# Performance work log

Measured on AMD Instinct MI355X. Metric: run time of the kernel, lower is better.

Reference implementation:

```python
import jax, jax.numpy as jnp
import numpy as np

B, S, D, H, DH = 1, 4096, 768, 12, 64
BS = 64            # block size
NB = S // BS       # 64 blocks
R = 3              # random blocks per query block
L = 2              # encoder layers
V = 50358          # vocab
F = 3072           # ffn hidden
C = 8              # num labels
EPS = 1e-12


def _ln(x, w, b):
    mu = jnp.mean(x, -1, keepdims=True)
    var = jnp.var(x, -1, keepdims=True)
    return (x - mu) * jax.lax.rsqrt(var + EPS) * w + b


def _bigbird_attn(x, rand, Wq, bq, Wk, bk, Wv, bv, Wo, bo):
    # x: [B,S,D]; rand: [H,NB,R] int block indices
    def split(h):  # -> [B,H,NB,BS,DH]
        return h.reshape(B, NB, BS, H, DH).transpose(0, 3, 1, 2, 4)
    q = split(x @ Wq + bq)
    k = split(x @ Wk + bk)
    v = split(x @ Wv + bv)
    scale = 1.0 / np.sqrt(DH).astype(np.float32)
    kf = k.reshape(B, H, S, DH)
    vf = v.reshape(B, H, S, DH)
    # global (first/last) query blocks attend to everything
    qe = q[:, :, jnp.array([0, NB - 1])]                       # [B,H,2,BS,DH]
    se = jnp.einsum('bhnqd,bhkd->bhnqk', qe, kf) * scale       # [B,H,2,BS,S]
    oe = jnp.einsum('bhnqk,bhkd->bhnqd', jax.nn.softmax(se, -1), vf)
    # middle query blocks: global(0, NB-1) + sliding window + R random blocks
    mid = jnp.arange(1, NB - 1)                                # [M]
    win = jnp.stack([jnp.zeros_like(mid), jnp.full_like(mid, NB - 1),
                     mid - 1, mid, mid + 1], -1)               # [M,5]
    band = jnp.concatenate([jnp.broadcast_to(win, (H, NB - 2, 5)),
                            rand[:, 1:NB - 1]], -1)            # [H,M,W]
    Wn = band.shape[-1]
    hidx = jnp.arange(H)[:, None, None]
    kb = k[:, hidx, band].reshape(B, H, NB - 2, Wn * BS, DH)
    vb = v[:, hidx, band].reshape(B, H, NB - 2, Wn * BS, DH)
    sm = jnp.einsum('bhmqd,bhmkd->bhmqk', q[:, :, 1:NB - 1], kb) * scale
    om = jnp.einsum('bhmqk,bhmkd->bhmqd', jax.nn.softmax(sm, -1), vb)
    o = jnp.concatenate([oe[:, :, 0:1], om, oe[:, :, 1:2]], 2)  # [B,H,NB,BS,DH]
    o = o.transpose(0, 2, 3, 1, 4).reshape(B, S, D)
    return o @ Wo + bo


def _forward(input_ids, rand_attn, word_emb, pos_emb, emb_ln_w, emb_ln_b,
             Wq, bq, Wk, bk, Wv, bv, Wo, bo, ln1_w, ln1_b,
             W1, b1, W2, b2, ln2_w, ln2_b, Wc, bc):
    h = word_emb[input_ids] + pos_emb[None, :S]
    h = _ln(h, emb_ln_w, emb_ln_b)
    for l in range(L):
        a = _bigbird_attn(h, rand_attn[l], Wq[l], bq[l], Wk[l], bk[l],
                          Wv[l], bv[l], Wo[l], bo[l])
        h = _ln(h + a, ln1_w[l], ln1_b[l])
        f = jax.nn.gelu(h @ W1[l] + b1[l], approximate=True) @ W2[l] + b2[l]
        h = _ln(h + f, ln2_w[l], ln2_b[l])
    return h[:, -1, :] @ Wc + bc   # [B, C]


def setup_inputs() -> dict:
    key = jax.random.key(0)
    ks = jax.random.split(key, 24)
    std = 0.02
    d = {
        'input_ids': jax.random.randint(ks[0], (B, S), 0, V, dtype=jnp.int32),
        'rand_attn': jax.random.randint(ks[1], (L, H, NB, R), 0, NB, dtype=jnp.int32),
        'word_emb': jax.random.normal(ks[2], (V, D), jnp.float32) * std,
        'pos_emb': jax.random.normal(ks[3], (S, D), jnp.float32) * std,
        'emb_ln_w': jnp.ones((D,), jnp.float32),
        'emb_ln_b': jnp.zeros((D,), jnp.float32),
        'Wq': jax.random.normal(ks[4], (L, D, D), jnp.float32) * std,
        'bq': jnp.zeros((L, D), jnp.float32),
        'Wk': jax.random.normal(ks[5], (L, D, D), jnp.float32) * std,
        'bk': jnp.zeros((L, D), jnp.float32),
        'Wv': jax.random.normal(ks[6], (L, D, D), jnp.float32) * std,
        'bv': jnp.zeros((L, D), jnp.float32),
        'Wo': jax.random.normal(ks[7], (L, D, D), jnp.float32) * std,
        'bo': jnp.zeros((L, D), jnp.float32),
        'ln1_w': jnp.ones((L, D), jnp.float32),
        'ln1_b': jnp.zeros((L, D), jnp.float32),
        'W1': jax.random.normal(ks[8], (L, D, F), jnp.float32) * std,
        'b1': jnp.zeros((L, F), jnp.float32),
        'W2': jax.random.normal(ks[9], (L, F, D), jnp.float32) * std,
        'b2': jnp.zeros((L, D), jnp.float32),
        'ln2_w': jnp.ones((L, D), jnp.float32),
        'ln2_b': jnp.zeros((L, D), jnp.float32),
        'Wc': jax.random.normal(ks[10], (D, C), jnp.float32) * std,
        'bc': jnp.zeros((C,), jnp.float32),
    }
    return d


def reference(input_ids, rand_attn, word_emb, pos_emb, emb_ln_w, emb_ln_b,
              Wq, bq, Wk, bk, Wv, bv, Wo, bo, ln1_w, ln1_b,
              W1, b1, W2, b2, ln2_w, ln2_b, Wc, bc):
    return _forward(input_ids, rand_attn, word_emb, pos_emb, emb_ln_w, emb_ln_b,
                    Wq, bq, Wk, bk, Wv, bv, Wo, bo, ln1_w, ln1_b,
                    W1, b1, W2, b2, ln2_w, ln2_b, Wc, bc)
```

## Files before the change

kernel.cpp:

```cpp
#include <hip/hip_runtime.h>
#include <stdint.h>

#define S_LEN 4096
#define DMODEL 768
#define NHEAD 12
#define DHEAD 64
#define NBLK 64
#define FF 3072
#define NLAYER 2
#define NMID (NHEAD * (NBLK - 2))
#define NEDGE_WG (NHEAD * 2 * 8)

typedef __attribute__((ext_vector_type(8))) short short8;
typedef __attribute__((ext_vector_type(4))) float floatx4;
typedef unsigned short ushort_t;

__device__ __forceinline__ unsigned short f2bf(float f) {
    union { float f; unsigned u; } v; v.f = f;
    unsigned r = v.u + 0x7FFFu + ((v.u >> 16) & 1u);
    return (unsigned short)(r >> 16);
}

__device__ __forceinline__ void load_lds16(const void* g, void* l) {
    __builtin_amdgcn_global_load_lds((const __attribute__((address_space(1))) void*)g,
                                     (__attribute__((address_space(3))) void*)l, 16, 0, 0);
}

__global__ void embed_ln_kernel(const int* __restrict__ ids, const float* __restrict__ wemb,
                                const float* __restrict__ pemb, const float* __restrict__ w,
                                const float* __restrict__ b, float* __restrict__ hf,
                                ushort_t* __restrict__ hb) {
    int s = blockIdx.x, t = threadIdx.x;
    const float* we = wemb + (size_t)ids[s] * DMODEL;
    const float* pe = pemb + (size_t)s * DMODEL;
    float x0 = we[t] + pe[t];
    float x1 = we[t + 256] + pe[t + 256];
    float x2 = we[t + 512] + pe[t + 512];
    float sum = x0 + x1 + x2;
    float sum2 = x0 * x0 + x1 * x1 + x2 * x2;
    __shared__ float sred[8];
    for (int o = 32; o >= 1; o >>= 1) { sum += __shfl_down(sum, o); sum2 += __shfl_down(sum2, o); }
    if ((t & 63) == 0) { sred[t >> 6] = sum; sred[4 + (t >> 6)] = sum2; }
    __syncthreads();
    float ts = sred[0] + sred[1] + sred[2] + sred[3];
    float ts2 = sred[4] + sred[5] + sred[6] + sred[7];
    float mu = ts * (1.0f / DMODEL);
    float rs = rsqrtf(ts2 * (1.0f / DMODEL) - mu * mu + 1e-12f);
    size_t base = (size_t)s * DMODEL;
    float y0 = (x0 - mu) * rs * w[t] + b[t];
    float y1 = (x1 - mu) * rs * w[t + 256] + b[t + 256];
    float y2 = (x2 - mu) * rs * w[t + 512] + b[t + 512];
    hf[base + t] = y0; hf[base + t + 256] = y1; hf[base + t + 512] = y2;
    hb[base + t] = f2bf(y0); hb[base + t + 256] = f2bf(y1); hb[base + t + 512] = f2bf(y2);
}

__global__ void ln_kernel(const float* __restrict__ in, const float* __restrict__ w,
                          const float* __restrict__ b, float* __restrict__ hf,
                          ushort_t* __restrict__ hb) {
    int s = blockIdx.x, t = threadIdx.x;
    const float* row = in + (size_t)s * DMODEL;
    float x0 = row[t], x1 = row[t + 256], x2 = row[t + 512];
    float sum = x0 + x1 + x2;
    float sum2 = x0 * x0 + x1 * x1 + x2 * x2;
    __shared__ float sred[8];
    for (int o = 32; o >= 1; o >>= 1) { sum += __shfl_down(sum, o); sum2 += __shfl_down(sum2, o); }
    if ((t & 63) == 0) { sred[t >> 6] = sum; sred[4 + (t >> 6)] = sum2; }
    __syncthreads();
    float ts = sred[0] + sred[1] + sred[2] + sred[3];
    float ts2 = sred[4] + sred[5] + sred[6] + sred[7];
    float mu = ts * (1.0f / DMODEL);
    float rs = rsqrtf(ts2 * (1.0f / DMODEL) - mu * mu + 1e-12f);
    size_t base = (size_t)s * DMODEL;
    float y0 = (x0 - mu) * rs * w[t] + b[t];
    float y1 = (x1 - mu) * rs * w[t + 256] + b[t + 256];
    float y2 = (x2 - mu) * rs * w[t + 512] + b[t + 512];
    hf[base + t] = y0; hf[base + t + 256] = y1; hf[base + t + 512] = y2;
    hb[base + t] = f2bf(y0); hb[base + t + 256] = f2bf(y1); hb[base + t + 512] = f2bf(y2);
}

__global__ void transpose_cvt(const float* __restrict__ src, ushort_t* __restrict__ dst,
                              int K, int N) {
    __shared__ float tile[32][33];
    int n0 = blockIdx.x * 32, k0 = blockIdx.y * 32;
    int tx = threadIdx.x, ty = threadIdx.y;
    for (int i = 0; i < 32; i += 8)
        tile[ty + i][tx] = src[(size_t)(k0 + ty + i) * N + n0 + tx];
    __syncthreads();
    for (int i = 0; i < 32; i += 8)
        dst[(size_t)(n0 + ty + i) * K + k0 + tx] = f2bf(tile[tx][ty + i]);
}

template <int MODE>
__global__ __launch_bounds__(256, 2) void gemm_bf16(
    const ushort_t* __restrict__ A, const ushort_t* __restrict__ BT,
    int M, int N, int K,
    const float* __restrict__ bias, const float* __restrict__ resid,
    float* __restrict__ outf, ushort_t* __restrict__ outb,
    ushort_t* __restrict__ qout, ushort_t* __restrict__ kout, ushort_t* __restrict__ vout,
    const float* __restrict__ bq, const float* __restrict__ bk, const float* __restrict__ bv) {
    __shared__ __align__(16) ushort_t Asm[128 * 32];
    __shared__ __align__(16) ushort_t Bsm[128 * 32];
    int tid = threadIdx.x;
    int lane = tid & 63, wave = tid >> 6;
    int quad = lane >> 4, l16 = lane & 15;
    int wm = wave >> 1, wn = wave & 1;
    long arow0 = (long)blockIdx.y * 128;
    long bcol0 = (long)blockIdx.x * 128;
    int rr = lane >> 2;
    int gchunk = (lane & 3) ^ (rr & 3) ^ ((rr >> 2) & 3);
    const ushort_t* agp0 = A + (arow0 + rr) * (long)K + gchunk * 8;
    const ushort_t* bgp0 = BT + (bcol0 + rr) * (long)K + gchunk * 8;
    int sl = quad ^ (l16 & 3) ^ ((l16 >> 2) & 3);
    floatx4 acc[4][4];
#pragma unroll
    for (int i = 0; i < 4; i++)
#pragma unroll
        for (int j = 0; j < 4; j++) acc[i][j] = (floatx4){0.f, 0.f, 0.f, 0.f};

    for (int k0 = 0; k0 < K; k0 += 32) {
        __syncthreads();
#pragma unroll
        for (int t2 = 0; t2 < 2; t2++) {
            int seg = wave * 2 + t2;
            load_lds16(agp0 + (long)seg * 16 * K + k0, Asm + seg * 512);
            load_lds16(bgp0 + (long)seg * 16 * K + k0, Bsm + seg * 512);
        }
        __syncthreads();
        short8 af[4], bfv[4];
#pragma unroll
        for (int i = 0; i < 4; i++)
            af[i] = *(const short8*)&Asm[(wm * 64 + i * 16 + l16) * 32 + sl * 8];
#pragma unroll
        for (int j = 0; j < 4; j++)
            bfv[j] = *(const short8*)&Bsm[(wn * 64 + j * 16 + l16) * 32 + sl * 8];
#pragma unroll
        for (int i = 0; i < 4; i++)
#pragma unroll
            for (int j = 0; j < 4; j++)
                acc[i][j] = __builtin_amdgcn_mfma_f32_16x16x32_bf16(af[i], bfv[j], acc[i][j], 0, 0, 0);
    }

#pragma unroll
    for (int i = 0; i < 4; i++) {
        long row = arow0 + wm * 64 + i * 16 + quad * 4;
#pragma unroll
        for (int j = 0; j < 4; j++) {
            long col = bcol0 + wn * 64 + j * 16 + l16;
#pragma unroll
            for (int r = 0; r < 4; r++) {
                float v = acc[i][j][r];
                long rw = row + r;
                if (MODE == 0) {
                    int n = (int)col;
                    if (n < DMODEL) {
                        v = (v + bq[n]) * 0.125f;
                        int hh = n >> 6, dh = n & 63;
                        qout[((long)hh * S_LEN + rw) * DHEAD + dh] = f2bf(v);
                    } else if (n < 2 * DMODEL) {
                        int n2 = n - DMODEL; v += bk[n2];
                        int hh = n2 >> 6, dh = n2 & 63;
                        kout[((long)hh * S_LEN + rw) * DHEAD + dh] = f2bf(v);
                    } else {
                        int n2 = n - 2 * DMODEL; v += bv[n2];
                        int hh = n2 >> 6, dh = n2 & 63;
                        vout[((long)hh * S_LEN + rw) * DHEAD + dh] = f2bf(v);
                    }
                } else if (MODE == 1) {
                    v += bias[col] + resid[rw * (long)N + col];
                    outf[rw * (long)N + col] = v;
                } else {
                    v += bias[col];
                    float u = 0.7978845608f * (v + 0.044715f * v * v * v);
                    v = 0.5f * v * (1.0f + tanhf(u));
                    outb[rw * (long)N + col] = f2bf(v);
                }
            }
        }
    }
}

__global__ __launch_bounds__(256, 2) void attn_kernel(
    const ushort_t* __restrict__ qb, const ushort_t* __restrict__ kb,
    const ushort_t* __restrict__ vb, const int* __restrict__ randl,
    ushort_t* __restrict__ out, float* __restrict__ opart, float* __restrict__ mlpart) {
    __shared__ __align__(16) ushort_t Ks[64 * 72];
    __shared__ __align__(16) ushort_t Vs[64 * 72];
    __shared__ __align__(16) ushort_t Ps[4][16 * 72];
    __shared__ int kls[8];
    int tid = threadIdx.x, lane = tid & 63, wave = tid >> 6, quad = lane >> 4, l16 = lane & 15;
    int g = blockIdx.x;
    int h, qblk, chunk = 0, eidx = 0;
    bool mid;
    if (g < NMID) {
        mid = true;
        h = g / (NBLK - 2);
        qblk = 1 + g % (NBLK - 2);
    } else {
        mid = false;
        int t = g - NMID;
        int side = t / (NHEAD * 8);
        int t2 = t % (NHEAD * 8);
        h = t2 >> 3;
        chunk = t2 & 7;
        qblk = side ? (NBLK - 1) : 0;
        eidx = side * NHEAD + h;
    }
    if (mid && tid < 8) {
        int v;
        if (tid == 0) v = 0;
        else if (tid == 1) v = NBLK - 1;
        else if (tid == 2) v = qblk - 1;
        else if (tid == 3) v = qblk;
        else if (tid == 4) v = qblk + 1;
        else v = randl[(h * NBLK + qblk) * 3 + (tid - 5)];
        kls[tid] = v;
    }
    const ushort_t* qh = qb + (size_t)h * S_LEN * DHEAD;
    const ushort_t* kh = kb + (size_t)h * S_LEN * DHEAD;
    const ushort_t* vh = vb + (size_t)h * S_LEN * DHEAD;
    size_t qoff = ((size_t)(qblk * 64 + wave * 16 + l16)) * DHEAD;
    short8 qf0 = *(const short8*)&qh[qoff + quad * 8];
    short8 qf1 = *(const short8*)&qh[qoff + 32 + quad * 8];
    floatx4 oacc[4];
#pragma unroll
    for (int j = 0; j < 4; j++) oacc[j] = (floatx4){0.f, 0.f, 0.f, 0.f};
    float mrun[4] = {-1e30f, -1e30f, -1e30f, -1e30f};
    float lrun[4] = {0.f, 0.f, 0.f, 0.f};

    for (int it = 0; it < 8; ++it) {
        __syncthreads();
        int kbi = mid ? kls[it] : (chunk * 8 + it);
        {
            const ushort_t* src = kh + (size_t)kbi * 64 * DHEAD;
#pragma unroll
            for (int c = 0; c < 2; c++) {
                int chk = tid + c * 256;
                int krow = chk >> 3, kc = chk & 7;
                *(uint4*)&Ks[krow * 72 + kc * 8] = *(const uint4*)&src[chk * 8];
            }
            const ushort_t* vsrc = vh + (size_t)kbi * 64 * DHEAD;
#pragma unroll
            for (int c = 0; c < 2; c++) {
                int dh0 = wave * 16 + c * 8;
                uint4 d4 = *(const uint4*)&vsrc[lane * DHEAD + dh0];
                const ushort_t* e = (const ushort_t*)&d4;
#pragma unroll
                for (int j = 0; j < 8; j++) Vs[(dh0 + j) * 72 + lane] = e[j];
            }
        }
        __syncthreads();
        floatx4 sacc[4];
#pragma unroll
        for (int jt = 0; jt < 4; jt++) {
            short8 kf0 = *(const short8*)&Ks[(jt * 16 + l16) * 72 + quad * 8];
            short8 kf1 = *(const short8*)&Ks[(jt * 16 + l16) * 72 + 32 + quad * 8];
            floatx4 z = (floatx4){0.f, 0.f, 0.f, 0.f};
            z = __builtin_amdgcn_mfma_f32_16x16x32_bf16(qf0, kf0, z, 0, 0, 0);
            z = __builtin_amdgcn_mfma_f32_16x16x32_bf16(qf1, kf1, z, 0, 0, 0);
            sacc[jt] = z;
        }
#pragma unroll
        for (int r = 0; r < 4; r++) {
            float mx = fmaxf(fmaxf(sacc[0][r], sacc[1][r]), fmaxf(sacc[2][r], sacc[3][r]));
#pragma unroll
            for (int o = 1; o < 16; o <<= 1) mx = fmaxf(mx, __shfl_xor(mx, o));
            float mnew = fmaxf(mrun[r], mx);
            float al = __expf(mrun[r] - mnew);
            float pv[4], ps = 0.f;
#pragma unroll
            for (int jt = 0; jt < 4; jt++) { pv[jt] = __expf(sacc[jt][r] - mnew); ps += pv[jt]; }
#pragma unroll
            for (int o = 1; o < 16; o <<= 1) ps += __shfl_xor(ps, o);
            lrun[r] = lrun[r] * al + ps;
            mrun[r] = mnew;
#pragma unroll
            for (int jt = 0; jt < 4; jt++) {
                oacc[jt][r] *= al;
                Ps[wave][(quad * 4 + r) * 72 + jt * 16 + l16] = f2bf(pv[jt]);
            }
        }
        short8 pa0 = *(const short8*)&Ps[wave][l16 * 72 + quad * 8];
        short8 pa1 = *(const short8*)&Ps[wave][l16 * 72 + 32 + quad * 8];
#pragma unroll
        for (int jt = 0; jt < 4; jt++) {
            short8 vf0 = *(const short8*)&Vs[(jt * 16 + l16) * 72 + quad * 8];
            short8 vf1 = *(const short8*)&Vs[(jt * 16 + l16) * 72 + 32 + quad * 8];
            oacc[jt] = __builtin_amdgcn_mfma_f32_16x16x32_bf16(pa0, vf0, oacc[jt], 0, 0, 0);
            oacc[jt] = __builtin_amdgcn_mfma_f32_16x16x32_bf16(pa1, vf1, oacc[jt], 0, 0, 0);
        }
    }
    if (mid) {
#pragma unroll
        for (int jt = 0; jt < 4; jt++)
#pragma unroll
            for (int r = 0; r < 4; r++) {
                int row = qblk * 64 + wave * 16 + quad * 4 + r;
                int col = h * DHEAD + jt * 16 + l16;
                out[(size_t)row * DMODEL + col] = f2bf(oacc[jt][r] / lrun[r]);
            }
    } else {
        float* op = opart + ((size_t)(eidx * 8 + chunk)) * 64 * 64;
        float* ml = mlpart + ((size_t)(eidx * 8 + chunk)) * 64 * 2;
#pragma unroll
        for (int jt = 0; jt < 4; jt++)
#pragma unroll
            for (int r = 0; r < 4; r++) {
                int row = wave * 16 + quad * 4 + r;
                op[(size_t)row * 64 + jt * 16 + l16] = oacc[jt][r];
            }
        if (l16 == 0) {
#pragma unroll
            for (int r = 0; r < 4; r++) {
                int row = wave * 16 + quad * 4 + r;
                ml[row * 2 + 0] = mrun[r];
                ml[row * 2 + 1] = lrun[r];
            }
        }
    }
}

__global__ void attn_combine(const float* __restrict__ opart, const float* __restrict__ mlpart,
                             ushort_t* __restrict__ out) {
    int e = blockIdx.x;
    int side = e / NHEAD, h = e % NHEAD;
    int qblk = side ? (NBLK - 1) : 0;
    __shared__ float mls[8][64][2];
    int tid = threadIdx.x;
    for (int i = tid; i < 8 * 64 * 2; i += 256)
        ((float*)mls)[i] = mlpart[(size_t)e * 8 * 64 * 2 + i];
    __syncthreads();
    int col = tid & 63, r0 = (tid >> 6) * 16;
    const float* ope = opart + (size_t)e * 8 * 64 * 64;
    for (int row = r0; row < r0 + 16; ++row) {
        float M = -1e30f;
#pragma unroll
        for (int p = 0; p < 8; p++) M = fmaxf(M, mls[p][row][0]);
        float L = 0.f, O = 0.f;
#pragma unroll
        for (int p = 0; p < 8; p++) {
            float al = __expf(mls[p][row][0] - M);
            L += mls[p][row][1] * al;
            O += ope[((size_t)p * 64 + row) * 64 + col] * al;
        }
        out[(size_t)(qblk * 64 + row) * DMODEL + h * DHEAD + col] = f2bf(O / L);
    }
}

__global__ void classifier_kernel(const float* __restrict__ hf, const float* __restrict__ Wc,
                                  const float* __restrict__ bc, float* __restrict__ out) {
    int t = threadIdx.x;
    int c = t & 7, seg = t >> 3;
    const float* hr = hf + (size_t)(S_LEN - 1) * DMODEL;
    float p = 0.f;
    for (int i = 0; i < 24; i++) { int d = seg * 24 + i; p += hr[d] * Wc[d * 8 + c]; }
    __shared__ float red[256];
    red[t] = p;
    __syncthreads();
    for (int o = 128; o >= 8; o >>= 1) { if (t < o) red[t] += red[t + o]; __syncthreads(); }
    if (t < 8) out[t] = red[t] + bc[t];
}

extern "C" void kernel_launch(void* const* d_in, const int* in_sizes, int n_in,
                              void* d_out, int out_size, void* d_ws, size_t ws_size,
                              hipStream_t stream) {
    (void)in_sizes; (void)n_in; (void)out_size; (void)ws_size;
    const int* input_ids = (const int*)d_in[0];
    const int* rand_attn = (const int*)d_in[1];
    const float* word_emb = (const float*)d_in[2];
    const float* pos_emb = (const float*)d_in[3];
    const float* emb_ln_w = (const float*)d_in[4];
    const float* emb_ln_b = (const float*)d_in[5];
    const float* Wq = (const float*)d_in[6];
    const float* bq = (const float*)d_in[7];
    const float* Wk = (const float*)d_in[8];
    const float* bk = (const float*)d_in[9];
    const float* Wv = (const float*)d_in[10];
    const float* bv = (const float*)d_in[11];
    const float* Wo = (const float*)d_in[12];
    const float* bo = (const float*)d_in[13];
    const float* ln1_w = (const float*)d_in[14];
    const float* ln1_b = (const float*)d_in[15];
    const float* W1 = (const float*)d_in[16];
    const float* b1 = (const float*)d_in[17];
    const float* W2 = (const float*)d_in[18];
    const float* b2 = (const float*)d_in[19];
    const float* ln2_w = (const float*)d_in[20];
    const float* ln2_b = (const float*)d_in[21];
    const float* Wc = (const float*)d_in[22];
    const float* bc = (const float*)d_in[23];
    float* outp = (float*)d_out;

    char* ws = (char*)d_ws;
    size_t off = 0;
    auto alloc = [&](size_t bytes) -> void* {
        void* p = ws + off;
        off += (bytes + 255) & ~(size_t)255;
        return p;
    };
    float* hf = (float*)alloc((size_t)S_LEN * DMODEL * 4);
    ushort_t* hb = (ushort_t*)alloc((size_t)S_LEN * DMODEL * 2);
    float* res = (float*)alloc((size_t)S_LEN * DMODEL * 4);
    ushort_t* WqkvT = (ushort_t*)alloc((size_t)3 * DMODEL * DMODEL * 2);
    ushort_t* WoT = (ushort_t*)alloc((size_t)DMODEL * DMODEL * 2);
    ushort_t* W1T = (ushort_t*)alloc((size_t)FF * DMODEL * 2);
    ushort_t* W2T = (ushort_t*)alloc((size_t)DMODEL * FF * 2);
    ushort_t* qbuf = (ushort_t*)alloc((size_t)NHEAD * S_LEN * DHEAD * 2);
    ushort_t* kbuf = (ushort_t*)alloc((size_t)NHEAD * S_LEN * DHEAD * 2);
    ushort_t* vbuf = (ushort_t*)alloc((size_t)NHEAD * S_LEN * DHEAD * 2);
    ushort_t* attnb = (ushort_t*)alloc((size_t)S_LEN * DMODEL * 2);
    ushort_t* gbuf = (ushort_t*)alloc((size_t)S_LEN * FF * 2);
    float* opart = (float*)alloc((size_t)24 * 8 * 64 * 64 * 4);
    float* mlpart = (float*)alloc((size_t)24 * 8 * 64 * 2 * 4);

    dim3 blk256(256);
    dim3 tb(32, 8);

    embed_ln_kernel<<<S_LEN, blk256, 0, stream>>>(input_ids, word_emb, pos_emb,
                                                  emb_ln_w, emb_ln_b, hf, hb);

    for (int l = 0; l < NLAYER; ++l) {
        const float* Wq_l = Wq + (size_t)l * DMODEL * DMODEL;
        const float* Wk_l = Wk + (size_t)l * DMODEL * DMODEL;
        const float* Wv_l = Wv + (size_t)l * DMODEL * DMODEL;
        const float* Wo_l = Wo + (size_t)l * DMODEL * DMODEL;
        const float* W1_l = W1 + (size_t)l * DMODEL * FF;
        const float* W2_l = W2 + (size_t)l * FF * DMODEL;
        const float* bq_l = bq + (size_t)l * DMODEL;
        const float* bk_l = bk + (size_t)l * DMODEL;
        const float* bv_l = bv + (size_t)l * DMODEL;
        const float* bo_l = bo + (size_t)l * DMODEL;
        const float* b1_l = b1 + (size_t)l * FF;
        const float* b2_l = b2 + (size_t)l * DMODEL;
        const float* ln1w_l = ln1_w + (size_t)l * DMODEL;
        const float* ln1b_l = ln1_b + (size_t)l * DMODEL;
        const float* ln2w_l = ln2_w + (size_t)l * DMODEL;
        const float* ln2b_l = ln2_b + (size_t)l * DMODEL;
        const int* rand_l = rand_attn + (size_t)l * NHEAD * NBLK * 3;

        transpose_cvt<<<dim3(DMODEL / 32, DMODEL / 32), tb, 0, stream>>>(Wq_l, WqkvT, DMODEL, DMODEL);
        transpose_cvt<<<dim3(DMODEL / 32, DMODEL / 32), tb, 0, stream>>>(Wk_l, WqkvT + (size_t)DMODEL * DMODEL, DMODEL, DMODEL);
        transpose_cvt<<<dim3(DMODEL / 32, DMODEL / 32), tb, 0, stream>>>(Wv_l, WqkvT + (size_t)2 * DMODEL * DMODEL, DMODEL, DMODEL);
        transpose_cvt<<<dim3(DMODEL / 32, DMODEL / 32), tb, 0, stream>>>(Wo_l, WoT, DMODEL, DMODEL);
        transpose_cvt<<<dim3(FF / 32, DMODEL / 32), tb, 0, stream>>>(W1_l, W1T, DMODEL, FF);
        transpose_cvt<<<dim3(DMODEL / 32, FF / 32), tb, 0, stream>>>(W2_l, W2T, FF, DMODEL);

        gemm_bf16<0><<<dim3(3 * DMODEL / 128, S_LEN / 128), blk256, 0, stream>>>(
            hb, WqkvT, S_LEN, 3 * DMODEL, DMODEL,
            nullptr, nullptr, nullptr, nullptr, qbuf, kbuf, vbuf, bq_l, bk_l, bv_l);

        attn_kernel<<<NMID + NEDGE_WG, blk256, 0, stream>>>(qbuf, kbuf, vbuf, rand_l,
                                                            attnb, opart, mlpart);
        attn_combine<<<24, blk256, 0, stream>>>(opart, mlpart, attnb);

        gemm_bf16<1><<<dim3(DMODEL / 128, S_LEN / 128), blk256, 0, stream>>>(
            attnb, WoT, S_LEN, DMODEL, DMODEL,
            bo_l, hf, res, nullptr, nullptr, nullptr, nullptr, nullptr, nullptr, nullptr);

        ln_kernel<<<S_LEN, blk256, 0, stream>>>(res, ln1w_l, ln1b_l, hf, hb);

        gemm_bf16<2><<<dim3(FF / 128, S_LEN / 128), blk256, 0, stream>>>(
            hb, W1T, S_LEN, FF, DMODEL,
            b1_l, nullptr, nullptr, gbuf, nullptr, nullptr, nullptr, nullptr, nullptr, nullptr);

        gemm_bf16<1><<<dim3(DMODEL / 128, S_LEN / 128), blk256, 0, stream>>>(
            gbuf, W2T, S_LEN, DMODEL, FF,
            b2_l, hf, res, nullptr, nullptr, nullptr, nullptr, nullptr, nullptr, nullptr);

        ln_kernel<<<S_LEN, blk256, 0, stream>>>(res, ln2w_l, ln2b_l, hf, hb);
    }

    classifier_kernel<<<1, blk256, 0, stream>>>(hf, Wc, bc, outp);
}
```

Before: 737.3 us.

## Deepen GEMM K-tile to 64, merge weight transposes, use exp-based GELU

The bf16 GEMM now stages 64-wide K slices in LDS with an 8-way XOR swizzle and runs two MFMA sub-steps per barrier pair. This halves the number of sync rounds and doubles the LDS footprint. The six per-layer weight transpose launches are merged into one kernel launch to cut launch overhead. The GELU epilogue swaps tanhf for an __expf-based tanh, which is cheaper but slightly less accurate.

```diff
diff --git a/kernel.cpp b/kernel.cpp
--- a/kernel.cpp
+++ b/kernel.cpp
@@ -19,6 +19,13 @@
     union { float f; unsigned u; } v; v.f = f;
     unsigned r = v.u + 0x7FFFu + ((v.u >> 16) & 1u);
     return (unsigned short)(r >> 16);
+}
+
+__device__ __forceinline__ float fast_gelu(float v) {
+    float u = 0.7978845608f * (v + 0.044715f * v * v * v);
+    float e = __expf(2.0f * u);
+    float th = 1.0f - 2.0f / (e + 1.0f);
+    return 0.5f * v * (1.0f + th);
 }
 
 __device__ __forceinline__ void load_lds16(const void* g, void* l) {
@@ -78,10 +85,26 @@
     hb[base + t] = f2bf(y0); hb[base + t + 256] = f2bf(y1); hb[base + t + 512] = f2bf(y2);
 }
 
-__global__ void transpose_cvt(const float* __restrict__ src, ushort_t* __restrict__ dst,
-                              int K, int N) {
+__global__ void transpose_all(const float* __restrict__ Wq, const float* __restrict__ Wk,
+                              const float* __restrict__ Wv, const float* __restrict__ Wo,
+                              const float* __restrict__ W1, const float* __restrict__ W2,
+                              ushort_t* __restrict__ WqkvT, ushort_t* __restrict__ WoT,
+                              ushort_t* __restrict__ W1T, ushort_t* __restrict__ W2T) {
     __shared__ float tile[32][33];
-    int n0 = blockIdx.x * 32, k0 = blockIdx.y * 32;
+    int b = blockIdx.x;
+    const float* src; ushort_t* dst; int K, N, bx;
+    if (b < 2304) {
+        int m = b / 576, r = b % 576;
+        src = (m == 0) ? Wq : (m == 1) ? Wk : (m == 2) ? Wv : Wo;
+        dst = (m < 3) ? (WqkvT + (size_t)m * DMODEL * DMODEL) : WoT;
+        K = DMODEL; N = DMODEL; bx = r;
+    } else if (b < 4608) {
+        src = W1; dst = W1T; K = DMODEL; N = FF; bx = b - 2304;
+    } else {
+        src = W2; dst = W2T; K = FF; N = DMODEL; bx = b - 4608;
+    }
+    int gx = N / 32;
+    int n0 = (bx % gx) * 32, k0 = (bx / gx) * 32;
     int tx = threadIdx.x, ty = threadIdx.y;
     for (int i = 0; i < 32; i += 8)
         tile[ty + i][tx] = src[(size_t)(k0 + ty + i) * N + n0 + tx];
@@ -98,46 +121,50 @@
     float* __restrict__ outf, ushort_t* __restrict__ outb,
     ushort_t* __restrict__ qout, ushort_t* __restrict__ kout, ushort_t* __restrict__ vout,
     const float* __restrict__ bq, const float* __restrict__ bk, const float* __restrict__ bv) {
-    __shared__ __align__(16) ushort_t Asm[128 * 32];
-    __shared__ __align__(16) ushort_t Bsm[128 * 32];
+    __shared__ __align__(16) ushort_t Asm[128 * 64];
+    __shared__ __align__(16) ushort_t Bsm[128 * 64];
     int tid = threadIdx.x;
     int lane = tid & 63, wave = tid >> 6;
     int quad = lane >> 4, l16 = lane & 15;
     int wm = wave >> 1, wn = wave & 1;
     long arow0 = (long)blockIdx.y * 128;
     long bcol0 = (long)blockIdx.x * 128;
-    int rr = lane >> 2;
-    int gchunk = (lane & 3) ^ (rr & 3) ^ ((rr >> 2) & 3);
-    const ushort_t* agp0 = A + (arow0 + rr) * (long)K + gchunk * 8;
-    const ushort_t* bgp0 = BT + (bcol0 + rr) * (long)K + gchunk * 8;
-    int sl = quad ^ (l16 & 3) ^ ((l16 >> 2) & 3);
+    int r8 = lane >> 3;
+    int gchunk = (lane & 7) ^ (r8 & 7);
+    const ushort_t* agp0 = A + (arow0 + r8) * (long)K + gchunk * 8;
+    const ushort_t* bgp0 = BT + (bcol0 + r8) * (long)K + gchunk * 8;
     floatx4 acc[4][4];
 #pragma unroll
     for (int i = 0; i < 4; i++)
 #pragma unroll
         for (int j = 0; j < 4; j++) acc[i][j] = (floatx4){0.f, 0.f, 0.f, 0.f};
 
-    for (int k0 = 0; k0 < K; k0 += 32) {
+    for (int k0 = 0; k0 < K; k0 += 64) {
         __syncthreads();
 #pragma unroll
-        for (int t2 = 0; t2 < 2; t2++) {
-            int seg = wave * 2 + t2;
-            load_lds16(agp0 + (long)seg * 16 * K + k0, Asm + seg * 512);
-            load_lds16(bgp0 + (long)seg * 16 * K + k0, Bsm + seg * 512);
+        for (int t2 = 0; t2 < 4; t2++) {
+            int seg = wave * 4 + t2;
+            load_lds16(agp0 + (long)seg * 8 * K + k0, Asm + seg * 512);
+            load_lds16(bgp0 + (long)seg * 8 * K + k0, Bsm + seg * 512);
         }
         __syncthreads();
-        short8 af[4], bfv[4];
-#pragma unroll
-        for (int i = 0; i < 4; i++)
-            af[i] = *(const short8*)&Asm[(wm * 64 + i * 16 + l16) * 32 + sl * 8];
-#pragma unroll
-        for (int j = 0; j < 4; j++)
-            bfv[j] = *(const short8*)&Bsm[(wn * 64 + j * 16 + l16) * 32 + sl * 8];
-#pragma unroll
-        for (int i = 0; i < 4; i++)
+#pragma unroll
+        for (int ks = 0; ks < 2; ks++) {
+            short8 af[4], bfv[4];
+#pragma unroll
+            for (int i = 0; i < 4; i++)
+                af[i] = *(const short8*)&Asm[(wm * 64 + i * 16 + l16) * 64 +
+                                             (((ks * 4 + quad) ^ (l16 & 7)) * 8)];
 #pragma unroll
             for (int j = 0; j < 4; j++)
-                acc[i][j] = __builtin_amdgcn_mfma_f32_16x16x32_bf16(af[i], bfv[j], acc[i][j], 0, 0, 0);
+                bfv[j] = *(const short8*)&Bsm[(wn * 64 + j * 16 + l16) * 64 +
+                                              (((ks * 4 + quad) ^ (l16 & 7)) * 8)];
+#pragma unroll
+            for (int i = 0; i < 4; i++)
+#pragma unroll
+                for (int j = 0; j < 4; j++)
+                    acc[i][j] = __builtin_amdgcn_mfma_f32_16x16x32_bf16(af[i], bfv[j], acc[i][j], 0, 0, 0);
+        }
     }
 
 #pragma unroll
@@ -170,9 +197,7 @@
                     outf[rw * (long)N + col] = v;
                 } else {
                     v += bias[col];
-                    float u = 0.7978845608f * (v + 0.044715f * v * v * v);
-                    v = 0.5f * v * (1.0f + tanhf(u));
-                    outb[rw * (long)N + col] = f2bf(v);
+                    outb[rw * (long)N + col] = f2bf(fast_gelu(v));
                 }
             }
         }
@@ -437,12 +462,8 @@
         const float* ln2b_l = ln2_b + (size_t)l * DMODEL;
         const int* rand_l = rand_attn + (size_t)l * NHEAD * NBLK * 3;
 
-        transpose_cvt<<<dim3(DMODEL / 32, DMODEL / 32), tb, 0, stream>>>(Wq_l, WqkvT, DMODEL, DMODEL);
-        transpose_cvt<<<dim3(DMODEL / 32, DMODEL / 32), tb, 0, stream>>>(Wk_l, WqkvT + (size_t)DMODEL * DMODEL, DMODEL, DMODEL);
-        transpose_cvt<<<dim3(DMODEL / 32, DMODEL / 32), tb, 0, stream>>>(Wv_l, WqkvT + (size_t)2 * DMODEL * DMODEL, DMODEL, DMODEL);
-        transpose_cvt<<<dim3(DMODEL / 32, DMODEL / 32), tb, 0, stream>>>(Wo_l, WoT, DMODEL, DMODEL);
-        transpose_cvt<<<dim3(FF / 32, DMODEL / 32), tb, 0, stream>>>(W1_l, W1T, DMODEL, FF);
-        transpose_cvt<<<dim3(DMODEL / 32, FF / 32), tb, 0, stream>>>(W2_l, W2T, FF, DMODEL);
+        transpose_all<<<6912, tb, 0, stream>>>(Wq_l, Wk_l, Wv_l, Wo_l, W1_l, W2_l,
+                                               WqkvT, WoT, W1T, W2T);
 
         gemm_bf16<0><<<dim3(3 * DMODEL / 128, S_LEN / 128), blk256, 0, stream>>>(
             hb, WqkvT, S_LEN, 3 * DMODEL, DMODEL,
```

After: 680.4 us. 1.08x faster.
